# Optimization experiments

Measured on AMD Instinct MI355X. Metric: run time of the kernel, lower is better.

The kernel has to match this reference:

```python
import jax, jax.numpy as jnp
import numpy as np
import math

N, C3, T = 32, 192, 2048  # C3 = 3 * head_dim

def setup_inputs() -> dict:
    key = jax.random.key(0)
    qkv = jax.random.normal(key, (N, C3, T), dtype=jnp.float32)
    return {"qkv": qkv}

def reference(qkv):
    ch = qkv.shape[1] // 3
    q, k, v = jnp.split(qkv, 3, axis=1)              # each [N, C, T]
    scale = 1.0 / math.sqrt(math.sqrt(ch))           # applied to both q and k
    # [N, T, T] attention scores
    weight = jnp.einsum('bct,bcs->bts', q * scale, k * scale)
    weight = jax.nn.softmax(weight.astype(jnp.float32), axis=-1).astype(qkv.dtype)
    # [N, C, T] output
    return jnp.einsum('bts,bcs->bct', weight, v)
```

## Files before the change

kernel.cpp:

```cpp
#include <hip/hip_runtime.h>

#define T_DIM 2048
#define D_DIM 64
#define NB 32

#define KB_OFF 4194304
#define VB_OFF 8388608

typedef _Float16 half8 __attribute__((ext_vector_type(8)));
typedef _Float16 half4 __attribute__((ext_vector_type(4)));
typedef float f32x16 __attribute__((ext_vector_type(16)));
typedef float f32x4 __attribute__((ext_vector_type(4)));

#define ZERO16 (f32x16){0.f,0.f,0.f,0.f,0.f,0.f,0.f,0.f,0.f,0.f,0.f,0.f,0.f,0.f,0.f,0.f}

__global__ __launch_bounds__(256) void prepass(const float* __restrict__ qkv,
                                               _Float16* __restrict__ ws) {
  const int ttile = blockIdx.x;
  const int b = blockIdx.y;
  const int type = blockIdx.z + 1;
  const int t0 = ttile * 64;
  __shared__ float Ls[64][65];

  const int tid = threadIdx.x;
  const int cc = tid >> 4;
  const int tt = (tid & 15) << 2;
  const float* src = qkv + ((size_t)b * 192 + type * 64) * T_DIM;
#pragma unroll
  for (int p = 0; p < 4; ++p) {
    const int c = p * 16 + cc;
    float4 v = *(const float4*)&src[(size_t)c * T_DIM + t0 + tt];
    Ls[c][tt] = v.x; Ls[c][tt + 1] = v.y; Ls[c][tt + 2] = v.z; Ls[c][tt + 3] = v.w;
  }
  __syncthreads();

  if (type == 1) {
    const int f = tid >> 6, h = (tid >> 5) & 1, s31 = tid & 31;
    const int u = (s31 >> 2) & 3;
    const int m31 = s31 ^ ((((u ^ (u >> 1)) & 1) != 0) ? 12 : 0);
#pragma unroll
    for (int sbl = 0; sbl < 2; ++sbl) {
      const int sb = (t0 >> 5) + sbl;
      half8 hv;
#pragma unroll
      for (int j = 0; j < 8; ++j) hv[j] = (_Float16)Ls[f * 16 + h * 8 + j][sbl * 32 + s31];
      _Float16* dst = ws + KB_OFF + ((size_t)b * 64 + sb) * 2048 + f * 512 + h * 256 + m31 * 8;
      *(half8*)dst = hv;
    }
  } else {
#pragma unroll
    for (int p = 0; p < 2; ++p) {
      const int g = p * 256 + tid;
      const int sgl = g >> 6, c = g & 63;
      half8 hv;
#pragma unroll
      for (int j = 0; j < 8; ++j) hv[j] = (_Float16)Ls[c][sgl * 8 + j];
      _Float16* dst = ws + VB_OFF + (((size_t)b * 256 + (t0 >> 3) + sgl) * 64 + c) * 8;
      *(half8*)dst = hv;
    }
  }
}

__global__ __launch_bounds__(256, 2) void qkv_main(const float* __restrict__ qkv,
                                                   const _Float16* __restrict__ ws,
                                                   float* __restrict__ out) {
  const int tid = threadIdx.x;
  const int wave = tid >> 6, lane = tid & 63;
  const int l31 = lane & 31, h = lane >> 5;
  const int b = blockIdx.x & 31;
  const int qg = blockIdx.x >> 5;
  const int t0 = qg * 128 + wave * 32;

  const _Float16* kbase = ws + KB_OFF + (size_t)b * 131072;
  const _Float16* vbase = ws + VB_OFF + (size_t)b * 131072;

  const float QS = 0.125f * 1.4426950408889634f;
  const float* qsrc = qkv + (size_t)b * 192 * T_DIM + t0 + l31;
  half8 bq[4];
#pragma unroll
  for (int f = 0; f < 4; ++f)
#pragma unroll
    for (int j = 0; j < 8; ++j)
      bq[f][j] = (_Float16)(qsrc[(size_t)(f * 16 + h * 8 + j) * T_DIM] * QS);

  const f32x16 fz = ZERO16;
  f32x16 o0 = ZERO16, o1 = ZERO16;
  float lp = 0.f;

  const _Float16* kp = kbase + h * 256 + l31 * 8;
  const _Float16* vp = vbase + h * 512 + l31 * 8;

  half8 ak[4], bv[4];
#pragma unroll
  for (int f = 0; f < 4; ++f) ak[f] = *(const half8*)(kp + f * 512);
  bv[0] = *(const half8*)(vp);
  bv[1] = *(const half8*)(vp + 256);
  bv[2] = *(const half8*)(vp + 1024);
  bv[3] = *(const half8*)(vp + 1280);

#pragma unroll 2
  for (int sb = 0; sb < 64; ++sb) {
    const size_t nxt = (size_t)(sb + 1 < 64 ? sb + 1 : sb) * 2048;
    const _Float16* kn = kp + nxt;
    half8 an0 = *(const half8*)(kn);
    half8 an1 = *(const half8*)(kn + 512);
    half8 an2 = *(const half8*)(kn + 1024);
    half8 an3 = *(const half8*)(kn + 1536);
    const _Float16* vn = vp + nxt;
    half8 bn0 = *(const half8*)(vn);
    half8 bn1 = *(const half8*)(vn + 256);
    half8 bn2 = *(const half8*)(vn + 1024);
    half8 bn3 = *(const half8*)(vn + 1280);

    f32x16 s;
    s = __builtin_amdgcn_mfma_f32_32x32x16_f16(ak[0], bq[0], fz, 0, 0, 0);
    s = __builtin_amdgcn_mfma_f32_32x32x16_f16(ak[1], bq[1], s, 0, 0, 0);
    s = __builtin_amdgcn_mfma_f32_32x32x16_f16(ak[2], bq[2], s, 0, 0, 0);
    s = __builtin_amdgcn_mfma_f32_32x32x16_f16(ak[3], bq[3], s, 0, 0, 0);

    float es[16];
#pragma unroll
    for (int g = 0; g < 16; ++g) es[g] = __builtin_amdgcn_exp2f(s[g]);
    lp += (((es[0] + es[1]) + (es[2] + es[3])) + ((es[4] + es[5]) + (es[6] + es[7]))) +
          (((es[8] + es[9]) + (es[10] + es[11])) + ((es[12] + es[13]) + (es[14] + es[15])));

    half8 A0, A1;
#pragma unroll
    for (int j = 0; j < 8; ++j) A0[j] = (_Float16)es[j];
#pragma unroll
    for (int j = 0; j < 8; ++j) A1[j] = (_Float16)es[8 + j];

    o0 = __builtin_amdgcn_mfma_f32_32x32x16_f16(A0, bv[0], o0, 0, 0, 0);
    o1 = __builtin_amdgcn_mfma_f32_32x32x16_f16(A0, bv[1], o1, 0, 0, 0);
    o0 = __builtin_amdgcn_mfma_f32_32x32x16_f16(A1, bv[2], o0, 0, 0, 0);
    o1 = __builtin_amdgcn_mfma_f32_32x32x16_f16(A1, bv[3], o1, 0, 0, 0);

    ak[0] = an0; ak[1] = an1; ak[2] = an2; ak[3] = an3;
    bv[0] = bn0; bv[1] = bn1; bv[2] = bn2; bv[3] = bn3;
  }

  const float lf = lp + __shfl_xor(lp, 32);
  const float linv = 1.0f / lf;
  float* ob = out + (size_t)b * D_DIM * T_DIM;
#pragma unroll
  for (int g = 0; g < 4; ++g) {
    f32x4 r0, r1;
#pragma unroll
    for (int j = 0; j < 4; ++j) {
      const float il = __shfl(linv, g * 8 + h * 4 + j);
      r0[j] = o0[g * 4 + j] * il;
      r1[j] = o1[g * 4 + j] * il;
    }
    const int q = t0 + g * 8 + h * 4;
    *(f32x4*)&ob[(size_t)l31 * T_DIM + q] = r0;
    *(f32x4*)&ob[(size_t)(32 + l31) * T_DIM + q] = r1;
  }
}

extern "C" void kernel_launch(void* const* d_in, const int* in_sizes, int n_in,
                              void* d_out, int out_size, void* d_ws, size_t ws_size,
                              hipStream_t stream) {
  const float* qkv = (const float*)d_in[0];
  float* out = (float*)d_out;
  _Float16* ws = (_Float16*)d_ws;
  hipLaunchKernelGGL(prepass, dim3(32, 32, 2), dim3(256), 0, stream, qkv, ws);
  hipLaunchKernelGGL(qkv_main, dim3(512), dim3(256), 0, stream, qkv, ws, out);
}
```

Before: 127.6 us.

## Process two 32-query tiles per wave to reuse loaded K/V fragments

Each wave now covers 64 queries (two 32-row tiles) instead of 32. The K and V fragments loaded per key block feed both tiles, which halves global/L2 fetch traffic per unit of work. Blocks shrink to 2 waves (128 threads) so the grid keeps the same query coverage. The cost is about double the accumulator and Q registers per wave, plus fewer waves in flight to hide latency.

```diff
diff --git a/kernel.cpp b/kernel.cpp
--- a/kernel.cpp
+++ b/kernel.cpp
@@ -61,7 +61,7 @@
   }
 }
 
-__global__ __launch_bounds__(256, 2) void qkv_main(const float* __restrict__ qkv,
+__global__ __launch_bounds__(128, 1) void qkv_main(const float* __restrict__ qkv,
                                                    const _Float16* __restrict__ ws,
                                                    float* __restrict__ out) {
   const int tid = threadIdx.x;
@@ -69,23 +69,27 @@
   const int l31 = lane & 31, h = lane >> 5;
   const int b = blockIdx.x & 31;
   const int qg = blockIdx.x >> 5;
-  const int t0 = qg * 128 + wave * 32;
+  const int t0w = qg * 128 + wave * 64;
 
   const _Float16* kbase = ws + KB_OFF + (size_t)b * 131072;
   const _Float16* vbase = ws + VB_OFF + (size_t)b * 131072;
 
   const float QS = 0.125f * 1.4426950408889634f;
-  const float* qsrc = qkv + (size_t)b * 192 * T_DIM + t0 + l31;
-  half8 bq[4];
+  const float* qsA = qkv + (size_t)b * 192 * T_DIM + t0w + l31;
+  const float* qsB = qsA + 32;
+  half8 bqA[4], bqB[4];
 #pragma unroll
   for (int f = 0; f < 4; ++f)
 #pragma unroll
-    for (int j = 0; j < 8; ++j)
-      bq[f][j] = (_Float16)(qsrc[(size_t)(f * 16 + h * 8 + j) * T_DIM] * QS);
+    for (int j = 0; j < 8; ++j) {
+      const size_t off = (size_t)(f * 16 + h * 8 + j) * T_DIM;
+      bqA[f][j] = (_Float16)(qsA[off] * QS);
+      bqB[f][j] = (_Float16)(qsB[off] * QS);
+    }
 
   const f32x16 fz = ZERO16;
-  f32x16 o0 = ZERO16, o1 = ZERO16;
-  float lp = 0.f;
+  f32x16 oA0 = ZERO16, oA1 = ZERO16, oB0 = ZERO16, oB1 = ZERO16;
+  float lpA = 0.f, lpB = 0.f;
 
   const _Float16* kp = kbase + h * 256 + l31 * 8;
   const _Float16* vp = vbase + h * 512 + l31 * 8;
@@ -112,48 +116,89 @@
     half8 bn2 = *(const half8*)(vn + 1024);
     half8 bn3 = *(const half8*)(vn + 1280);
 
-    f32x16 s;
-    s = __builtin_amdgcn_mfma_f32_32x32x16_f16(ak[0], bq[0], fz, 0, 0, 0);
-    s = __builtin_amdgcn_mfma_f32_32x32x16_f16(ak[1], bq[1], s, 0, 0, 0);
-    s = __builtin_amdgcn_mfma_f32_32x32x16_f16(ak[2], bq[2], s, 0, 0, 0);
-    s = __builtin_amdgcn_mfma_f32_32x32x16_f16(ak[3], bq[3], s, 0, 0, 0);
-
-    float es[16];
-#pragma unroll
-    for (int g = 0; g < 16; ++g) es[g] = __builtin_amdgcn_exp2f(s[g]);
-    lp += (((es[0] + es[1]) + (es[2] + es[3])) + ((es[4] + es[5]) + (es[6] + es[7]))) +
-          (((es[8] + es[9]) + (es[10] + es[11])) + ((es[12] + es[13]) + (es[14] + es[15])));
-
-    half8 A0, A1;
-#pragma unroll
-    for (int j = 0; j < 8; ++j) A0[j] = (_Float16)es[j];
-#pragma unroll
-    for (int j = 0; j < 8; ++j) A1[j] = (_Float16)es[8 + j];
-
-    o0 = __builtin_amdgcn_mfma_f32_32x32x16_f16(A0, bv[0], o0, 0, 0, 0);
-    o1 = __builtin_amdgcn_mfma_f32_32x32x16_f16(A0, bv[1], o1, 0, 0, 0);
-    o0 = __builtin_amdgcn_mfma_f32_32x32x16_f16(A1, bv[2], o0, 0, 0, 0);
-    o1 = __builtin_amdgcn_mfma_f32_32x32x16_f16(A1, bv[3], o1, 0, 0, 0);
+    f32x16 sA;
+    sA = __builtin_amdgcn_mfma_f32_32x32x16_f16(ak[0], bqA[0], fz, 0, 0, 0);
+    sA = __builtin_amdgcn_mfma_f32_32x32x16_f16(ak[1], bqA[1], sA, 0, 0, 0);
+    sA = __builtin_amdgcn_mfma_f32_32x32x16_f16(ak[2], bqA[2], sA, 0, 0, 0);
+    sA = __builtin_amdgcn_mfma_f32_32x32x16_f16(ak[3], bqA[3], sA, 0, 0, 0);
+    f32x16 sB;
+    sB = __builtin_amdgcn_mfma_f32_32x32x16_f16(ak[0], bqB[0], fz, 0, 0, 0);
+    sB = __builtin_amdgcn_mfma_f32_32x32x16_f16(ak[1], bqB[1], sB, 0, 0, 0);
+    sB = __builtin_amdgcn_mfma_f32_32x32x16_f16(ak[2], bqB[2], sB, 0, 0, 0);
+    sB = __builtin_amdgcn_mfma_f32_32x32x16_f16(ak[3], bqB[3], sB, 0, 0, 0);
+
+    {
+      float es[16];
+#pragma unroll
+      for (int g = 0; g < 16; ++g) es[g] = __builtin_amdgcn_exp2f(sA[g]);
+      lpA += (((es[0] + es[1]) + (es[2] + es[3])) + ((es[4] + es[5]) + (es[6] + es[7]))) +
+             (((es[8] + es[9]) + (es[10] + es[11])) + ((es[12] + es[13]) + (es[14] + es[15])));
+      half8 A0, A1;
+#pragma unroll
+      for (int j = 0; j < 8; ++j) A0[j] = (_Float16)es[j];
+#pragma unroll
+      for (int j = 0; j < 8; ++j) A1[j] = (_Float16)es[8 + j];
+      oA0 = __builtin_amdgcn_mfma_f32_32x32x16_f16(A0, bv[0], oA0, 0, 0, 0);
+      oA1 = __builtin_amdgcn_mfma_f32_32x32x16_f16(A0, bv[1], oA1, 0, 0, 0);
+      oA0 = __builtin_amdgcn_mfma_f32_32x32x16_f16(A1, bv[2], oA0, 0, 0, 0);
+      oA1 = __builtin_amdgcn_mfma_f32_32x32x16_f16(A1, bv[3], oA1, 0, 0, 0);
+    }
+
+    {
+      float es[16];
+#pragma unroll
+      for (int g = 0; g < 16; ++g) es[g] = __builtin_amdgcn_exp2f(sB[g]);
+      lpB += (((es[0] + es[1]) + (es[2] + es[3])) + ((es[4] + es[5]) + (es[6] + es[7]))) +
+             (((es[8] + es[9]) + (es[10] + es[11])) + ((es[12] + es[13]) + (es[14] + es[15])));
+      half8 A0, A1;
+#pragma unroll
+      for (int j = 0; j < 8; ++j) A0[j] = (_Float16)es[j];
+#pragma unroll
+      for (int j = 0; j < 8; ++j) A1[j] = (_Float16)es[8 + j];
+      oB0 = __builtin_amdgcn_mfma_f32_32x32x16_f16(A0, bv[0], oB0, 0, 0, 0);
+      oB1 = __builtin_amdgcn_mfma_f32_32x32x16_f16(A0, bv[1], oB1, 0, 0, 0);
+      oB0 = __builtin_amdgcn_mfma_f32_32x32x16_f16(A1, bv[2], oB0, 0, 0, 0);
+      oB1 = __builtin_amdgcn_mfma_f32_32x32x16_f16(A1, bv[3], oB1, 0, 0, 0);
+    }
 
     ak[0] = an0; ak[1] = an1; ak[2] = an2; ak[3] = an3;
     bv[0] = bn0; bv[1] = bn1; bv[2] = bn2; bv[3] = bn3;
   }
 
-  const float lf = lp + __shfl_xor(lp, 32);
-  const float linv = 1.0f / lf;
   float* ob = out + (size_t)b * D_DIM * T_DIM;
-#pragma unroll
-  for (int g = 0; g < 4; ++g) {
-    f32x4 r0, r1;
-#pragma unroll
-    for (int j = 0; j < 4; ++j) {
-      const float il = __shfl(linv, g * 8 + h * 4 + j);
-      r0[j] = o0[g * 4 + j] * il;
-      r1[j] = o1[g * 4 + j] * il;
-    }
-    const int q = t0 + g * 8 + h * 4;
-    *(f32x4*)&ob[(size_t)l31 * T_DIM + q] = r0;
-    *(f32x4*)&ob[(size_t)(32 + l31) * T_DIM + q] = r1;
+  {
+    const float lf = lpA + __shfl_xor(lpA, 32);
+    const float linv = 1.0f / lf;
+#pragma unroll
+    for (int g = 0; g < 4; ++g) {
+      f32x4 r0, r1;
+#pragma unroll
+      for (int j = 0; j < 4; ++j) {
+        const float il = __shfl(linv, g * 8 + h * 4 + j);
+        r0[j] = oA0[g * 4 + j] * il;
+        r1[j] = oA1[g * 4 + j] * il;
+      }
+      const int q = t0w + g * 8 + h * 4;
+      *(f32x4*)&ob[(size_t)l31 * T_DIM + q] = r0;
+      *(f32x4*)&ob[(size_t)(32 + l31) * T_DIM + q] = r1;
+    }
+  }
+  {
+    const float lf = lpB + __shfl_xor(lpB, 32);
+    const float linv = 1.0f / lf;
+#pragma unroll
+    for (int g = 0; g < 4; ++g) {
+      f32x4 r0, r1;
+#pragma unroll
+      for (int j = 0; j < 4; ++j) {
+        const float il = __shfl(linv, g * 8 + h * 4 + j);
+        r0[j] = oB0[g * 4 + j] * il;
+        r1[j] = oB1[g * 4 + j] * il;
+      }
+      const int q = t0w + 32 + g * 8 + h * 4;
+      *(f32x4*)&ob[(size_t)l31 * T_DIM + q] = r0;
+      *(f32x4*)&ob[(size_t)(32 + l31) * T_DIM + q] = r1;
+    }
   }
 }
 
@@ -164,5 +209,5 @@
   float* out = (float*)d_out;
   _Float16* ws = (_Float16*)d_ws;
   hipLaunchKernelGGL(prepass, dim3(32, 32, 2), dim3(256), 0, stream, qkv, ws);
-  hipLaunchKernelGGL(qkv_main, dim3(512), dim3(256), 0, stream, qkv, ws, out);
+  hipLaunchKernelGGL(qkv_main, dim3(512), dim3(128), 0, stream, qkv, ws, out);
 }
```

New measurement: 138.7 us. +8.6%, slower.

## Software-pipeline QK and PV MFMAs on odd hardware wave slots

Applied to the files above, without the earlier changes.

Reads a hardware register (wave/SIMD slot id) and sends odd-slot waves down a software-pipelined loop: the PV MFMAs of the previous block are issued alongside the QK MFMAs of the current block, so the exp/convert work can overlap matrix-core execution. Even-slot waves keep the original loop, so waves sharing a SIMD run out of phase and interleave MFMA and VALU phases. This adds code size and register pressure, and depends on the meaning of the getreg field on this hardware.

```diff
diff --git a/kernel.cpp b/kernel.cpp
--- a/kernel.cpp
+++ b/kernel.cpp
@@ -8,7 +8,6 @@
 #define VB_OFF 8388608
 
 typedef _Float16 half8 __attribute__((ext_vector_type(8)));
-typedef _Float16 half4 __attribute__((ext_vector_type(4)));
 typedef float f32x16 __attribute__((ext_vector_type(16)));
 typedef float f32x4 __attribute__((ext_vector_type(4)));
 
@@ -90,53 +89,137 @@
   const _Float16* kp = kbase + h * 256 + l31 * 8;
   const _Float16* vp = vbase + h * 512 + l31 * 8;
 
-  half8 ak[4], bv[4];
-#pragma unroll
-  for (int f = 0; f < 4; ++f) ak[f] = *(const half8*)(kp + f * 512);
-  bv[0] = *(const half8*)(vp);
-  bv[1] = *(const half8*)(vp + 256);
-  bv[2] = *(const half8*)(vp + 1024);
-  bv[3] = *(const half8*)(vp + 1280);
+  const unsigned hwslot = __builtin_amdgcn_s_getreg(6148);
+
+  if ((hwslot & 1) == 0) {
+    half8 ak[4], bv[4];
+#pragma unroll
+    for (int f = 0; f < 4; ++f) ak[f] = *(const half8*)(kp + f * 512);
+    bv[0] = *(const half8*)(vp);
+    bv[1] = *(const half8*)(vp + 256);
+    bv[2] = *(const half8*)(vp + 1024);
+    bv[3] = *(const half8*)(vp + 1280);
 
 #pragma unroll 2
-  for (int sb = 0; sb < 64; ++sb) {
-    const size_t nxt = (size_t)(sb + 1 < 64 ? sb + 1 : sb) * 2048;
-    const _Float16* kn = kp + nxt;
-    half8 an0 = *(const half8*)(kn);
-    half8 an1 = *(const half8*)(kn + 512);
-    half8 an2 = *(const half8*)(kn + 1024);
-    half8 an3 = *(const half8*)(kn + 1536);
-    const _Float16* vn = vp + nxt;
-    half8 bn0 = *(const half8*)(vn);
-    half8 bn1 = *(const half8*)(vn + 256);
-    half8 bn2 = *(const half8*)(vn + 1024);
-    half8 bn3 = *(const half8*)(vn + 1280);
+    for (int sb = 0; sb < 64; ++sb) {
+      const size_t nxt = (size_t)(sb + 1 < 64 ? sb + 1 : sb) * 2048;
+      const _Float16* kn = kp + nxt;
+      half8 an0 = *(const half8*)(kn);
+      half8 an1 = *(const half8*)(kn + 512);
+      half8 an2 = *(const half8*)(kn + 1024);
+      half8 an3 = *(const half8*)(kn + 1536);
+      const _Float16* vn = vp + nxt;
+      half8 bn0 = *(const half8*)(vn);
+      half8 bn1 = *(const half8*)(vn + 256);
+      half8 bn2 = *(const half8*)(vn + 1024);
+      half8 bn3 = *(const half8*)(vn + 1280);
+
+      f32x16 s;
+      s = __builtin_amdgcn_mfma_f32_32x32x16_f16(ak[0], bq[0], fz, 0, 0, 0);
+      s = __builtin_amdgcn_mfma_f32_32x32x16_f16(ak[1], bq[1], s, 0, 0, 0);
+      s = __builtin_amdgcn_mfma_f32_32x32x16_f16(ak[2], bq[2], s, 0, 0, 0);
+      s = __builtin_amdgcn_mfma_f32_32x32x16_f16(ak[3], bq[3], s, 0, 0, 0);
+
+      float es[16];
+#pragma unroll
+      for (int g = 0; g < 16; ++g) es[g] = __builtin_amdgcn_exp2f(s[g]);
+      lp += (((es[0] + es[1]) + (es[2] + es[3])) + ((es[4] + es[5]) + (es[6] + es[7]))) +
+            (((es[8] + es[9]) + (es[10] + es[11])) + ((es[12] + es[13]) + (es[14] + es[15])));
+
+      half8 A0, A1;
+#pragma unroll
+      for (int j = 0; j < 8; ++j) A0[j] = (_Float16)es[j];
+#pragma unroll
+      for (int j = 0; j < 8; ++j) A1[j] = (_Float16)es[8 + j];
+
+      o0 = __builtin_amdgcn_mfma_f32_32x32x16_f16(A0, bv[0], o0, 0, 0, 0);
+      o1 = __builtin_amdgcn_mfma_f32_32x32x16_f16(A0, bv[1], o1, 0, 0, 0);
+      o0 = __builtin_amdgcn_mfma_f32_32x32x16_f16(A1, bv[2], o0, 0, 0, 0);
+      o1 = __builtin_amdgcn_mfma_f32_32x32x16_f16(A1, bv[3], o1, 0, 0, 0);
+
+      ak[0] = an0; ak[1] = an1; ak[2] = an2; ak[3] = an3;
+      bv[0] = bn0; bv[1] = bn1; bv[2] = bn2; bv[3] = bn3;
+    }
+  } else {
+    half8 akc0 = *(const half8*)(kp);
+    half8 akc1 = *(const half8*)(kp + 512);
+    half8 akc2 = *(const half8*)(kp + 1024);
+    half8 akc3 = *(const half8*)(kp + 1536);
+    half8 bvc0 = *(const half8*)(vp);
+    half8 bvc1 = *(const half8*)(vp + 256);
+    half8 bvc2 = *(const half8*)(vp + 1024);
+    half8 bvc3 = *(const half8*)(vp + 1280);
 
     f32x16 s;
-    s = __builtin_amdgcn_mfma_f32_32x32x16_f16(ak[0], bq[0], fz, 0, 0, 0);
-    s = __builtin_amdgcn_mfma_f32_32x32x16_f16(ak[1], bq[1], s, 0, 0, 0);
-    s = __builtin_amdgcn_mfma_f32_32x32x16_f16(ak[2], bq[2], s, 0, 0, 0);
-    s = __builtin_amdgcn_mfma_f32_32x32x16_f16(ak[3], bq[3], s, 0, 0, 0);
-
-    float es[16];
-#pragma unroll
-    for (int g = 0; g < 16; ++g) es[g] = __builtin_amdgcn_exp2f(s[g]);
-    lp += (((es[0] + es[1]) + (es[2] + es[3])) + ((es[4] + es[5]) + (es[6] + es[7]))) +
-          (((es[8] + es[9]) + (es[10] + es[11])) + ((es[12] + es[13]) + (es[14] + es[15])));
+    s = __builtin_amdgcn_mfma_f32_32x32x16_f16(akc0, bq[0], fz, 0, 0, 0);
+    s = __builtin_amdgcn_mfma_f32_32x32x16_f16(akc1, bq[1], s, 0, 0, 0);
+    s = __builtin_amdgcn_mfma_f32_32x32x16_f16(akc2, bq[2], s, 0, 0, 0);
+    s = __builtin_amdgcn_mfma_f32_32x32x16_f16(akc3, bq[3], s, 0, 0, 0);
+
+    half8 kn0 = *(const half8*)(kp + 2048);
+    half8 kn1 = *(const half8*)(kp + 2048 + 512);
+    half8 kn2 = *(const half8*)(kp + 2048 + 1024);
+    half8 kn3 = *(const half8*)(kp + 2048 + 1536);
+    half8 vn0 = *(const half8*)(vp + 2048);
+    half8 vn1 = *(const half8*)(vp + 2048 + 256);
+    half8 vn2 = *(const half8*)(vp + 2048 + 1024);
+    half8 vn3 = *(const half8*)(vp + 2048 + 1280);
 
     half8 A0, A1;
-#pragma unroll
-    for (int j = 0; j < 8; ++j) A0[j] = (_Float16)es[j];
-#pragma unroll
-    for (int j = 0; j < 8; ++j) A1[j] = (_Float16)es[8 + j];
-
-    o0 = __builtin_amdgcn_mfma_f32_32x32x16_f16(A0, bv[0], o0, 0, 0, 0);
-    o1 = __builtin_amdgcn_mfma_f32_32x32x16_f16(A0, bv[1], o1, 0, 0, 0);
-    o0 = __builtin_amdgcn_mfma_f32_32x32x16_f16(A1, bv[2], o0, 0, 0, 0);
-    o1 = __builtin_amdgcn_mfma_f32_32x32x16_f16(A1, bv[3], o1, 0, 0, 0);
-
-    ak[0] = an0; ak[1] = an1; ak[2] = an2; ak[3] = an3;
-    bv[0] = bn0; bv[1] = bn1; bv[2] = bn2; bv[3] = bn3;
+    {
+      float es[16];
+#pragma unroll
+      for (int g = 0; g < 16; ++g) es[g] = __builtin_amdgcn_exp2f(s[g]);
+      lp += (((es[0] + es[1]) + (es[2] + es[3])) + ((es[4] + es[5]) + (es[6] + es[7]))) +
+            (((es[8] + es[9]) + (es[10] + es[11])) + ((es[12] + es[13]) + (es[14] + es[15])));
+#pragma unroll
+      for (int j = 0; j < 8; ++j) A0[j] = (_Float16)es[j];
+#pragma unroll
+      for (int j = 0; j < 8; ++j) A1[j] = (_Float16)es[8 + j];
+    }
+
+#pragma unroll 2
+    for (int i = 1; i < 64; ++i) {
+      o0 = __builtin_amdgcn_mfma_f32_32x32x16_f16(A0, bvc0, o0, 0, 0, 0);
+      o1 = __builtin_amdgcn_mfma_f32_32x32x16_f16(A0, bvc1, o1, 0, 0, 0);
+      o0 = __builtin_amdgcn_mfma_f32_32x32x16_f16(A1, bvc2, o0, 0, 0, 0);
+      o1 = __builtin_amdgcn_mfma_f32_32x32x16_f16(A1, bvc3, o1, 0, 0, 0);
+
+      akc0 = kn0; akc1 = kn1; akc2 = kn2; akc3 = kn3;
+      bvc0 = vn0; bvc1 = vn1; bvc2 = vn2; bvc3 = vn3;
+
+      s = __builtin_amdgcn_mfma_f32_32x32x16_f16(akc0, bq[0], fz, 0, 0, 0);
+      s = __builtin_amdgcn_mfma_f32_32x32x16_f16(akc1, bq[1], s, 0, 0, 0);
+      s = __builtin_amdgcn_mfma_f32_32x32x16_f16(akc2, bq[2], s, 0, 0, 0);
+      s = __builtin_amdgcn_mfma_f32_32x32x16_f16(akc3, bq[3], s, 0, 0, 0);
+
+      const size_t ofn = (size_t)(i + 1 < 64 ? i + 1 : i) * 2048;
+      const _Float16* kn = kp + ofn;
+      kn0 = *(const half8*)(kn);
+      kn1 = *(const half8*)(kn + 512);
+      kn2 = *(const half8*)(kn + 1024);
+      kn3 = *(const half8*)(kn + 1536);
+      const _Float16* vn = vp + ofn;
+      vn0 = *(const half8*)(vn);
+      vn1 = *(const half8*)(vn + 256);
+      vn2 = *(const half8*)(vn + 1024);
+      vn3 = *(const half8*)(vn + 1280);
+
+      float es[16];
+#pragma unroll
+      for (int g = 0; g < 16; ++g) es[g] = __builtin_amdgcn_exp2f(s[g]);
+      lp += (((es[0] + es[1]) + (es[2] + es[3])) + ((es[4] + es[5]) + (es[6] + es[7]))) +
+            (((es[8] + es[9]) + (es[10] + es[11])) + ((es[12] + es[13]) + (es[14] + es[15])));
+#pragma unroll
+      for (int j = 0; j < 8; ++j) A0[j] = (_Float16)es[j];
+#pragma unroll
+      for (int j = 0; j < 8; ++j) A1[j] = (_Float16)es[8 + j];
+    }
+
+    o0 = __builtin_amdgcn_mfma_f32_32x32x16_f16(A0, bvc0, o0, 0, 0, 0);
+    o1 = __builtin_amdgcn_mfma_f32_32x32x16_f16(A0, bvc1, o1, 0, 0, 0);
+    o0 = __builtin_amdgcn_mfma_f32_32x32x16_f16(A1, bvc2, o0, 0, 0, 0);
+    o1 = __builtin_amdgcn_mfma_f32_32x32x16_f16(A1, bvc3, o1, 0, 0, 0);
   }
 
   const float lf = lp + __shfl_xor(lp, 32);
```

New measurement: 127.3 us. Within noise of the previous version (-0.3%).
